# Optimization experiments

Hardware: AMD Instinct MI355X
Metric: run time of the kernel (lower is better)

Reference implementation:

```python
import jax, jax.numpy as jnp
import numpy as np
import math

MAX_DEGREE = 8  # n_harmonics = (MAX_DEGREE+1)**2 = 81


def _real_sph_harm_all(theta, phi, L):
    """Real part of scipy's sph_harm(m, l, phi, theta) for all (l, m),
    l in [0, L], m in [-l, l], stacked on the last axis (81 terms for L=8).

    Uses the stable associated-Legendre recurrence (with Condon-Shortley
    phase, matching scipy) instead of a per-term CPU loop.
    """
    x = jnp.cos(theta)
    s = jnp.sin(theta)  # sin(theta) >= 0 since theta in [0, pi]

    # P[(l, m)] = associated Legendre P_l^m(cos theta), 0 <= m <= l <= L
    P = {}
    for m in range(L + 1):
        if m == 0:
            Pmm = jnp.ones_like(x)
        else:
            # P_m^m = -(2m-1) * sin(theta) * P_{m-1}^{m-1}  (Condon-Shortley)
            Pmm = -(2 * m - 1) * s * P[(m - 1, m - 1)]
        P[(m, m)] = Pmm
        if m + 1 <= L:
            P[(m + 1, m)] = (2 * m + 1) * x * Pmm
        for l in range(m + 2, L + 1):
            P[(l, m)] = ((2 * l - 1) * x * P[(l - 1, m)]
                         - (l + m - 1) * P[(l - 2, m)]) / (l - m)

    ys = []
    for l in range(L + 1):
        for m in range(-l, l + 1):
            am = abs(m)
            norm = math.sqrt((2 * l + 1) / (4.0 * math.pi)
                             * math.factorial(l - am) / math.factorial(l + am))
            # Re(Y_l^m) = N * P_l^{|m|}(cos th) * cos(|m| phi); for m<0 multiply
            # by (-1)^{|m|} since Y_l^{-m} = (-1)^m conj(Y_l^m) (scipy convention).
            Y = norm * P[(l, am)] * jnp.cos(am * phi)
            if m < 0:
                Y = Y * ((-1.0) ** am)
            ys.append(Y)
    return jnp.stack(ys, axis=-1)  # [batch, channels, (L+1)^2]


def setup_inputs() -> dict:
    key = jax.random.key(0)
    k1, k2 = jax.random.split(key)
    positions = jax.random.normal(k1, (32, 1024, 3), dtype=jnp.float32)
    harmonics_weights = jax.random.normal(k2, (81, 2048), dtype=jnp.float32)
    return {"positions": positions, "harmonics_weights": harmonics_weights}


def reference(positions, harmonics_weights):
    # normalize to unit sphere
    r = jnp.linalg.norm(positions, axis=-1, keepdims=True)
    pos = positions / (r + 1e-8)
    theta = jnp.arccos(jnp.clip(pos[..., 2], -1.0, 1.0))  # polar angle
    phi = jnp.arctan2(pos[..., 1], pos[..., 0])           # azimuth
    harmonics = _real_sph_harm_all(theta, phi, MAX_DEGREE)  # [B, C, 81]
    return jnp.matmul(harmonics, harmonics_weights)         # [B, C, 2048]
```

## Files before the change

kernel.cpp:

```cpp
#include <hip/hip_runtime.h>


typedef __attribute__((ext_vector_type(8))) short bf16x8;
typedef __attribute__((ext_vector_type(4))) float f32x4;

#define BM 128
#define BN 128
#define LDA 104
#define KPAD 96
#define LDSC 132

constexpr double PI_D = 3.14159265358979323846;
constexpr double csqrt_c(double v) {
  if (v <= 0.0) return 0.0;
  double g = v < 1.0 ? 1.0 : v;
  for (int i = 0; i < 100; ++i) g = 0.5 * (g + v / g);
  return g;
}
struct Norms { float c[81]; };
constexpr Norms make_norms() {
  Norms n{};
  for (int l = 0; l <= 8; ++l)
    for (int m = -l; m <= l; ++m) {
      int am = m < 0 ? -m : m;
      double fr = 1.0;
      for (int i = l - am + 1; i <= l + am; ++i) fr *= (double)i;
      double v = csqrt_c((2.0 * l + 1.0) / (4.0 * PI_D) / fr);
      if (m < 0 && (am & 1)) v = -v;
      n.c[l * l + l + m] = (float)v;
    }
  return n;
}
constexpr Norms NORMS = make_norms();

__device__ __forceinline__ unsigned f2bf(float f) {
  unsigned u = __float_as_uint(f);
  return (u + 0x7fffu + ((u >> 16) & 1u)) >> 16;
}

__global__ __launch_bounds__(256)
void wt_convert_kernel(const float* __restrict__ W, unsigned short* __restrict__ WT, int nch) {
  const int t = blockIdx.x * 256 + threadIdx.x;
  if (t >= nch * 12) return;
  const int kg = t / nch;
  const int c  = t - kg * nch;
  unsigned short v[8];
#pragma unroll
  for (int j = 0; j < 8; ++j) {
    const int k = kg * 8 + j;
    v[j] = (k < 81) ? (unsigned short)f2bf(W[(size_t)k * nch + c]) : (unsigned short)0;
  }
  unsigned* dst = reinterpret_cast<unsigned*>(WT + (size_t)c * KPAD + kg * 8);
#pragma unroll
  for (int j = 0; j < 4; ++j)
    dst[j] = (unsigned)v[2 * j] | ((unsigned)v[2 * j + 1] << 16);
}

__global__ __launch_bounds__(256)
void sph_mfma_kernel(const float* __restrict__ pos,
                     const unsigned short* __restrict__ WT,
                     float* __restrict__ out, int nch)
{
  __shared__ __align__(16) char smem[BM * LDSC * 4];
  unsigned short* H = reinterpret_cast<unsigned short*>(smem);
  float*          C = reinterpret_cast<float*>(smem);

  const int tid  = threadIdx.x;
  const int lane = tid & 63;
  const int wid  = tid >> 6;
  const int wc   = wid >> 1, wp = wid & 1;
  const int l15  = lane & 15, l4 = lane >> 4;
  const int mblk = blockIdx.y, nblk = blockIdx.x;

  if (tid < BM) {
    const int gp = mblk * BM + tid;
    const float px = pos[gp * 3 + 0];
    const float py = pos[gp * 3 + 1];
    const float pz = pos[gp * 3 + 2];
    const float r   = sqrtf(px * px + py * py + pz * pz);
    const float inv = 1.0f / (r + 1e-8f);
    const float xn = px * inv, yn = py * inv, zn = pz * inv;
    const float x = fminf(1.0f, fmaxf(-1.0f, zn));
    const float s = sqrtf(fmaxf(0.0f, 1.0f - x * x));
    const float rho = sqrtf(xn * xn + yn * yn);
    const float c1  = rho > 0.0f ? xn / rho : 1.0f;

    float cm[9];
    cm[0] = 1.0f; cm[1] = c1;
#pragma unroll
    for (int m = 2; m <= 8; ++m) cm[m] = 2.0f * c1 * cm[m - 1] - cm[m - 2];

    float P[9][9];
#pragma unroll
    for (int m = 0; m <= 8; ++m) {
      if (m == 0) P[0][0] = 1.0f;
      else        P[m][m] = -(float)(2 * m - 1) * s * P[m - 1][m - 1];
      if (m + 1 <= 8) P[m + 1][m] = (float)(2 * m + 1) * x * P[m][m];
#pragma unroll
      for (int l = m + 2; l <= 8; ++l)
        P[l][m] = ((float)(2 * l - 1) * x * P[l - 1][m]
                   - (float)(l + m - 1) * P[l - 2][m]) / (float)(l - m);
    }

    float y[KPAD];
#pragma unroll
    for (int l = 0; l <= 8; ++l)
#pragma unroll
      for (int m = -l; m <= l; ++m) {
        const int am  = m < 0 ? -m : m;
        const int idx = l * l + l + m;
        y[idx] = NORMS.c[idx] * P[l][am] * cm[am];
      }
#pragma unroll
    for (int i = 81; i < KPAD; ++i) y[i] = 0.0f;

    unsigned* hrow = reinterpret_cast<unsigned*>(&H[tid * LDA]);
#pragma unroll
    for (int i = 0; i < KPAD / 2; ++i)
      hrow[i] = f2bf(y[2 * i]) | (f2bf(y[2 * i + 1]) << 16);
  }

  bf16x8 wfrag[3][4];
  const unsigned short* wt_base =
      WT + (size_t)(nblk * BN + wc * 64 + l15) * KPAD + l4 * 8;
#pragma unroll
  for (int kk = 0; kk < 3; ++kk)
#pragma unroll
    for (int cmr = 0; cmr < 4; ++cmr)
      wfrag[kk][cmr] = *reinterpret_cast<const bf16x8*>(
          wt_base + (size_t)cmr * 16 * KPAD + kk * 32);

  __syncthreads();

  f32x4 acc[4][4] = {};
#pragma unroll
  for (int kk = 0; kk < 3; ++kk) {
    bf16x8 hfrag[4];
#pragma unroll
    for (int pn = 0; pn < 4; ++pn)
      hfrag[pn] = *reinterpret_cast<const bf16x8*>(
          &H[(wp * 64 + pn * 16 + l15) * LDA + kk * 32 + l4 * 8]);
#pragma unroll
    for (int cmr = 0; cmr < 4; ++cmr)
#pragma unroll
      for (int pn = 0; pn < 4; ++pn)
        acc[cmr][pn] = __builtin_amdgcn_mfma_f32_16x16x32_bf16(
            wfrag[kk][cmr], hfrag[pn], acc[cmr][pn], 0, 0, 0);
  }

  __syncthreads();

#pragma unroll
  for (int pn = 0; pn < 4; ++pn) {
    const int crow = wp * 64 + pn * 16 + l15;
#pragma unroll
    for (int cmr = 0; cmr < 4; ++cmr)
      *reinterpret_cast<f32x4*>(&C[crow * LDSC + wc * 64 + cmr * 16 + l4 * 4]) =
          acc[cmr][pn];
  }

  __syncthreads();

  const size_t obase = (size_t)(mblk * BM) * nch + (size_t)nblk * BN;
#pragma unroll
  for (int i = 0; i < 16; ++i) {
    const int f = i * 1024 + tid * 4;
    const int r = f >> 7;
    const int c = f & 127;
    const f32x4 v = *reinterpret_cast<const f32x4*>(&C[r * LDSC + c]);
    *reinterpret_cast<f32x4*>(out + obase + (size_t)r * nch + c) = v;
  }
}

extern "C" void kernel_launch(void* const* d_in, const int* in_sizes, int n_in,
                              void* d_out, int out_size, void* d_ws, size_t ws_size,
                              hipStream_t stream) {
  const float* pos = (const float*)d_in[0];
  const float* W   = (const float*)d_in[1];
  float*       out = (float*)d_out;
  const int npts = in_sizes[0] / 3;
  const int nch  = in_sizes[1] / 81;

  unsigned short* WT = (unsigned short*)d_ws;
  const int cvt_threads = nch * 12;
  wt_convert_kernel<<<(cvt_threads + 255) / 256, 256, 0, stream>>>(W, WT, nch);
  dim3 grid(nch / BN, npts / BM);
  sph_mfma_kernel<<<grid, 256, 0, stream>>>(pos, WT, out, nch);
}
```

Before: 55.45 us.

## Shrink epilogue LDS staging, remap workgroups across XCDs, cheapen trig math

The output epilogue now stages the accumulator tile through LDS in four 32-row slices, each followed by a synchronised store pass. That shrinks shared memory from about 66KB to the 26KB already needed for the harmonics tile, so more workgroups can be resident per CU. The grid becomes 1D with a swizzle that gives each XCD a contiguous run of tiles, and the division and sqrt in the harmonics setup are replaced by rsqrt and multiply-by-reciprocal. In exchange the epilogue gains extra barriers, and the kernel is mainly bound by writing the output.

After: 58.71 us. +5.9%, slower.

```diff
diff --git a/kernel.cpp b/kernel.cpp
--- a/kernel.cpp
+++ b/kernel.cpp
@@ -8,7 +8,7 @@
 #define BN 128
 #define LDA 104
 #define KPAD 96
-#define LDSC 132
+#define LDCC 132
 
 constexpr double PI_D = 3.14159265358979323846;
 constexpr double csqrt_c(double v) {
@@ -59,18 +59,23 @@
 __global__ __launch_bounds__(256)
 void sph_mfma_kernel(const float* __restrict__ pos,
                      const unsigned short* __restrict__ WT,
-                     float* __restrict__ out, int nch)
+                     float* __restrict__ out, int nch, int nbx)
 {
-  __shared__ __align__(16) char smem[BM * LDSC * 4];
+  __shared__ __align__(16) char smem[BM * LDA * 2];
   unsigned short* H = reinterpret_cast<unsigned short*>(smem);
   float*          C = reinterpret_cast<float*>(smem);
+
+  const int nwg  = gridDim.x;
+  const int orig = blockIdx.x;
+  const int wgid = ((nwg & 7) == 0) ? (orig & 7) * (nwg >> 3) + (orig >> 3) : orig;
+  const int mblk = wgid / nbx;
+  const int nblk = wgid - mblk * nbx;
 
   const int tid  = threadIdx.x;
   const int lane = tid & 63;
   const int wid  = tid >> 6;
   const int wc   = wid >> 1, wp = wid & 1;
   const int l15  = lane & 15, l4 = lane >> 4;
-  const int mblk = blockIdx.y, nblk = blockIdx.x;
 
   if (tid < BM) {
     const int gp = mblk * BM + tid;
@@ -82,8 +87,8 @@
     const float xn = px * inv, yn = py * inv, zn = pz * inv;
     const float x = fminf(1.0f, fmaxf(-1.0f, zn));
     const float s = sqrtf(fmaxf(0.0f, 1.0f - x * x));
-    const float rho = sqrtf(xn * xn + yn * yn);
-    const float c1  = rho > 0.0f ? xn / rho : 1.0f;
+    const float rho2 = xn * xn + yn * yn;
+    const float c1   = rho2 > 0.0f ? xn * rsqrtf(rho2) : 1.0f;
 
     float cm[9];
     cm[0] = 1.0f; cm[1] = c1;
@@ -99,7 +104,7 @@
 #pragma unroll
       for (int l = m + 2; l <= 8; ++l)
         P[l][m] = ((float)(2 * l - 1) * x * P[l - 1][m]
-                   - (float)(l + m - 1) * P[l - 2][m]) / (float)(l - m);
+                   - (float)(l + m - 1) * P[l - 2][m]) * (1.0f / (float)(l - m));
     }
 
     float y[KPAD];
@@ -150,25 +155,26 @@
 
   __syncthreads();
 
+  const size_t obase = (size_t)(mblk * BM) * nch + (size_t)nblk * BN;
 #pragma unroll
   for (int pn = 0; pn < 4; ++pn) {
-    const int crow = wp * 64 + pn * 16 + l15;
 #pragma unroll
     for (int cmr = 0; cmr < 4; ++cmr)
-      *reinterpret_cast<f32x4*>(&C[crow * LDSC + wc * 64 + cmr * 16 + l4 * 4]) =
-          acc[cmr][pn];
-  }
+      *reinterpret_cast<f32x4*>(
+          &C[(wp * 16 + l15) * LDCC + wc * 64 + cmr * 16 + l4 * 4]) = acc[cmr][pn];
+    __syncthreads();
 
-  __syncthreads();
-
-  const size_t obase = (size_t)(mblk * BM) * nch + (size_t)nblk * BN;
 #pragma unroll
-  for (int i = 0; i < 16; ++i) {
-    const int f = i * 1024 + tid * 4;
-    const int r = f >> 7;
-    const int c = f & 127;
-    const f32x4 v = *reinterpret_cast<const f32x4*>(&C[r * LDSC + c]);
-    *reinterpret_cast<f32x4*>(out + obase + (size_t)r * nch + c) = v;
+    for (int i = 0; i < 4; ++i) {
+      const int idx = (i * 256 + tid) * 4;
+      const int cr  = idx >> 7;
+      const int cc  = idx & 127;
+      const int wpg = cr >> 4;
+      const int lrow = wpg * 64 + pn * 16 + (cr & 15);
+      const f32x4 v = *reinterpret_cast<const f32x4*>(&C[cr * LDCC + cc]);
+      *reinterpret_cast<f32x4*>(out + obase + (size_t)lrow * nch + cc) = v;
+    }
+    if (pn < 3) __syncthreads();
   }
 }
 
@@ -184,6 +190,8 @@
   unsigned short* WT = (unsigned short*)d_ws;
   const int cvt_threads = nch * 12;
   wt_convert_kernel<<<(cvt_threads + 255) / 256, 256, 0, stream>>>(W, WT, nch);
-  dim3 grid(nch / BN, npts / BM);
-  sph_mfma_kernel<<<grid, 256, 0, stream>>>(pos, WT, out, nch);
+
+  const int nbx = nch / BN;
+  const int nwg = nbx * (npts / BM);
+  sph_mfma_kernel<<<nwg, 256, 0, stream>>>(pos, WT, out, nch, nbx);
 }
```

## Split harmonics into a separate kernel and stream GEMM directly from global

Applied to the files above, without the earlier changes.

The harmonics evaluation moves out of the GEMM kernel into its own kernel that writes padded bf16 rows to workspace. The GEMM kernel then loads both operands straight from global memory with no LDS staging. It also uses a 1D grid ordered M-fastest and a half-size output staging buffer written in two passes. The aim is to stop recomputing harmonics in every N-block (16x redundancy), take the transcendental-heavy work off the GEMM critical path, and raise occupancy through lower LDS use. The cost is an extra launch and an HG round trip, and the old fused path remains as a fallback when the workspace is too small.

New measurement: 61.38 us. 10.7% more time.

```diff
diff --git a/kernel.cpp b/kernel.cpp
--- a/kernel.cpp
+++ b/kernel.cpp
@@ -6,9 +6,9 @@
 
 #define BM 128
 #define BN 128
+#define KPAD 96
+#define LDCC 132
 #define LDA 104
-#define KPAD 96
-#define LDSC 132
 
 constexpr double PI_D = 3.14159265358979323846;
 constexpr double csqrt_c(double v) {
@@ -38,6 +38,44 @@
   return (u + 0x7fffu + ((u >> 16) & 1u)) >> 16;
 }
 
+__device__ __forceinline__ void harmonics96(float px, float py, float pz,
+                                            float* __restrict__ y) {
+  const float r   = sqrtf(px * px + py * py + pz * pz);
+  const float inv = 1.0f / (r + 1e-8f);
+  const float xn = px * inv, yn = py * inv, zn = pz * inv;
+  const float x = fminf(1.0f, fmaxf(-1.0f, zn));
+  const float s = sqrtf(fmaxf(0.0f, 1.0f - x * x));
+  const float rho = sqrtf(xn * xn + yn * yn);
+  const float c1  = rho > 0.0f ? xn / rho : 1.0f;
+
+  float cm[9];
+  cm[0] = 1.0f; cm[1] = c1;
+#pragma unroll
+  for (int m = 2; m <= 8; ++m) cm[m] = 2.0f * c1 * cm[m - 1] - cm[m - 2];
+
+  float P[9][9];
+#pragma unroll
+  for (int m = 0; m <= 8; ++m) {
+    if (m == 0) P[0][0] = 1.0f;
+    else        P[m][m] = -(float)(2 * m - 1) * s * P[m - 1][m - 1];
+    if (m + 1 <= 8) P[m + 1][m] = (float)(2 * m + 1) * x * P[m][m];
+#pragma unroll
+    for (int l = m + 2; l <= 8; ++l)
+      P[l][m] = ((float)(2 * l - 1) * x * P[l - 1][m]
+                 - (float)(l + m - 1) * P[l - 2][m]) / (float)(l - m);
+  }
+#pragma unroll
+  for (int l = 0; l <= 8; ++l)
+#pragma unroll
+    for (int m = -l; m <= l; ++m) {
+      const int am  = m < 0 ? -m : m;
+      const int idx = l * l + l + m;
+      y[idx] = NORMS.c[idx] * P[l][am] * cm[am];
+    }
+#pragma unroll
+  for (int i = 81; i < KPAD; ++i) y[i] = 0.0f;
+}
+
 __global__ __launch_bounds__(256)
 void wt_convert_kernel(const float* __restrict__ W, unsigned short* __restrict__ WT, int nch) {
   const int t = blockIdx.x * 256 + threadIdx.x;
@@ -57,11 +95,85 @@
 }
 
 __global__ __launch_bounds__(256)
-void sph_mfma_kernel(const float* __restrict__ pos,
-                     const unsigned short* __restrict__ WT,
-                     float* __restrict__ out, int nch)
+void harm_kernel(const float* __restrict__ pos, unsigned short* __restrict__ HG, int npts) {
+  const int t = blockIdx.x * 256 + threadIdx.x;
+  if (t >= npts) return;
+  float y[KPAD];
+  harmonics96(pos[t * 3 + 0], pos[t * 3 + 1], pos[t * 3 + 2], y);
+  unsigned* dst = reinterpret_cast<unsigned*>(HG + (size_t)t * KPAD);
+#pragma unroll
+  for (int i = 0; i < KPAD / 2; ++i)
+    dst[i] = f2bf(y[2 * i]) | (f2bf(y[2 * i + 1]) << 16);
+}
+
+__global__ __launch_bounds__(256)
+void gemm_kernel(const unsigned short* __restrict__ HG,
+                 const unsigned short* __restrict__ WT,
+                 float* __restrict__ out, int nch, int nmb)
 {
-  __shared__ __align__(16) char smem[BM * LDSC * 4];
+  __shared__ __align__(16) float C[64 * LDCC];
+  const int orig = blockIdx.x;
+  const int mblk = orig % nmb;
+  const int nblk = orig / nmb;
+
+  const int tid  = threadIdx.x;
+  const int lane = tid & 63;
+  const int wid  = tid >> 6;
+  const int wc   = wid >> 1, wp = wid & 1;
+  const int l15  = lane & 15, l4 = lane >> 4;
+
+  const unsigned short* hg_base = HG + (size_t)(mblk * BM + wp * 64 + l15) * KPAD + l4 * 8;
+  const unsigned short* wt_base = WT + (size_t)(nblk * BN + wc * 64 + l15) * KPAD + l4 * 8;
+
+  f32x4 acc[4][4] = {};
+#pragma unroll
+  for (int kk = 0; kk < 3; ++kk) {
+    bf16x8 wfrag[4], hfrag[4];
+#pragma unroll
+    for (int i = 0; i < 4; ++i)
+      wfrag[i] = *reinterpret_cast<const bf16x8*>(wt_base + (size_t)i * 16 * KPAD + kk * 32);
+#pragma unroll
+    for (int i = 0; i < 4; ++i)
+      hfrag[i] = *reinterpret_cast<const bf16x8*>(hg_base + (size_t)i * 16 * KPAD + kk * 32);
+#pragma unroll
+    for (int cmr = 0; cmr < 4; ++cmr)
+#pragma unroll
+      for (int pn = 0; pn < 4; ++pn)
+        acc[cmr][pn] = __builtin_amdgcn_mfma_f32_16x16x32_bf16(
+            wfrag[cmr], hfrag[pn], acc[cmr][pn], 0, 0, 0);
+  }
+
+  const size_t obase = (size_t)(mblk * BM) * nch + (size_t)nblk * BN;
+#pragma unroll
+  for (int h = 0; h < 2; ++h) {
+#pragma unroll
+    for (int q = 0; q < 2; ++q) {
+      const int lr = wp * 32 + q * 16 + l15;
+#pragma unroll
+      for (int cmr = 0; cmr < 4; ++cmr)
+        *reinterpret_cast<f32x4*>(&C[lr * LDCC + wc * 64 + cmr * 16 + l4 * 4]) =
+            acc[cmr][2 * h + q];
+    }
+    __syncthreads();
+#pragma unroll
+    for (int it = 0; it < 8; ++it) {
+      const int f  = it * 1024 + tid * 4;
+      const int lr = f >> 7;
+      const int cc = f & 127;
+      const int gr = (lr >> 5) * 64 + h * 32 + (lr & 31);
+      const f32x4 v = *reinterpret_cast<const f32x4*>(&C[lr * LDCC + cc]);
+      *reinterpret_cast<f32x4*>(out + obase + (size_t)gr * nch + cc) = v;
+    }
+    if (h == 0) __syncthreads();
+  }
+}
+
+__global__ __launch_bounds__(256)
+void sph_mfma_fused(const float* __restrict__ pos,
+                    const unsigned short* __restrict__ WT,
+                    float* __restrict__ out, int nch)
+{
+  __shared__ __align__(16) char smem[BM * LDCC * 4];
   unsigned short* H = reinterpret_cast<unsigned short*>(smem);
   float*          C = reinterpret_cast<float*>(smem);
 
@@ -74,46 +186,8 @@
 
   if (tid < BM) {
     const int gp = mblk * BM + tid;
-    const float px = pos[gp * 3 + 0];
-    const float py = pos[gp * 3 + 1];
-    const float pz = pos[gp * 3 + 2];
-    const float r   = sqrtf(px * px + py * py + pz * pz);
-    const float inv = 1.0f / (r + 1e-8f);
-    const float xn = px * inv, yn = py * inv, zn = pz * inv;
-    const float x = fminf(1.0f, fmaxf(-1.0f, zn));
-    const float s = sqrtf(fmaxf(0.0f, 1.0f - x * x));
-    const float rho = sqrtf(xn * xn + yn * yn);
-    const float c1  = rho > 0.0f ? xn / rho : 1.0f;
-
-    float cm[9];
-    cm[0] = 1.0f; cm[1] = c1;
-#pragma unroll
-    for (int m = 2; m <= 8; ++m) cm[m] = 2.0f * c1 * cm[m - 1] - cm[m - 2];
-
-    float P[9][9];
-#pragma unroll
-    for (int m = 0; m <= 8; ++m) {
-      if (m == 0) P[0][0] = 1.0f;
-      else        P[m][m] = -(float)(2 * m - 1) * s * P[m - 1][m - 1];
-      if (m + 1 <= 8) P[m + 1][m] = (float)(2 * m + 1) * x * P[m][m];
-#pragma unroll
-      for (int l = m + 2; l <= 8; ++l)
-        P[l][m] = ((float)(2 * l - 1) * x * P[l - 1][m]
-                   - (float)(l + m - 1) * P[l - 2][m]) / (float)(l - m);
-    }
-
     float y[KPAD];
-#pragma unroll
-    for (int l = 0; l <= 8; ++l)
-#pragma unroll
-      for (int m = -l; m <= l; ++m) {
-        const int am  = m < 0 ? -m : m;
-        const int idx = l * l + l + m;
-        y[idx] = NORMS.c[idx] * P[l][am] * cm[am];
-      }
-#pragma unroll
-    for (int i = 81; i < KPAD; ++i) y[i] = 0.0f;
-
+    harmonics96(pos[gp * 3 + 0], pos[gp * 3 + 1], pos[gp * 3 + 2], y);
     unsigned* hrow = reinterpret_cast<unsigned*>(&H[tid * LDA]);
 #pragma unroll
     for (int i = 0; i < KPAD / 2; ++i)
@@ -149,16 +223,14 @@
   }
 
   __syncthreads();
-
 #pragma unroll
   for (int pn = 0; pn < 4; ++pn) {
     const int crow = wp * 64 + pn * 16 + l15;
 #pragma unroll
     for (int cmr = 0; cmr < 4; ++cmr)
-      *reinterpret_cast<f32x4*>(&C[crow * LDSC + wc * 64 + cmr * 16 + l4 * 4]) =
+      *reinterpret_cast<f32x4*>(&C[crow * LDCC + wc * 64 + cmr * 16 + l4 * 4]) =
           acc[cmr][pn];
   }
-
   __syncthreads();
 
   const size_t obase = (size_t)(mblk * BM) * nch + (size_t)nblk * BN;
@@ -167,7 +239,7 @@
     const int f = i * 1024 + tid * 4;
     const int r = f >> 7;
     const int c = f & 127;
-    const f32x4 v = *reinterpret_cast<const f32x4*>(&C[r * LDSC + c]);
+    const f32x4 v = *reinterpret_cast<const f32x4*>(&C[r * LDCC + c]);
     *reinterpret_cast<f32x4*>(out + obase + (size_t)r * nch + c) = v;
   }
 }
@@ -181,9 +253,20 @@
   const int npts = in_sizes[0] / 3;
   const int nch  = in_sizes[1] / 81;
 
+  const size_t wt_bytes = (size_t)nch * KPAD * sizeof(unsigned short);
+  const size_t hg_bytes = (size_t)npts * KPAD * sizeof(unsigned short);
+
   unsigned short* WT = (unsigned short*)d_ws;
-  const int cvt_threads = nch * 12;
-  wt_convert_kernel<<<(cvt_threads + 255) / 256, 256, 0, stream>>>(W, WT, nch);
-  dim3 grid(nch / BN, npts / BM);
-  sph_mfma_kernel<<<grid, 256, 0, stream>>>(pos, WT, out, nch);
-}
+  wt_convert_kernel<<<(nch * 12 + 255) / 256, 256, 0, stream>>>(W, WT, nch);
+
+  if (ws_size >= wt_bytes + hg_bytes) {
+    unsigned short* HG = (unsigned short*)((char*)d_ws + wt_bytes);
+    harm_kernel<<<(npts + 255) / 256, 256, 0, stream>>>(pos, HG, npts);
+    const int nmb = npts / BM;
+    const int nwg = nmb * (nch / BN);
+    gemm_kernel<<<nwg, 256, 0, stream>>>(HG, WT, out, nch, nmb);
+  } else {
+    dim3 grid(nch / BN, npts / BM);
+    sph_mfma_fused<<<grid, 256, 0, stream>>>(pos, WT, out, nch);
+  }
+}
```
